# Kernel tuning notes

Hardware: AMD Instinct MI355X
Metric: run time of the kernel (lower is better)

## Reference

```python
import jax, jax.numpy as jnp
import numpy as np

H, W, C = 512, 512, 21
D_BI, D_SP = 5, 2
THETA_ALPHA, THETA_BETA, THETA_GAMMA = 80.0, 13.0, 3.0
BILATERAL_COMPAT, SPATIAL_COMPAT, COMPAT = 10.0, 3.0, -1.0
NUM_ITER = 5


def _build_lattice(feats):
    # Permutohedral lattice construction (Adams et al. 2010), vectorized numpy.
    # feats: [N, d] float64 -> (offsets [N,d+1] int32 into M lattice points,
    # barycentric weights [N,d+1] float32, blur_neighbors [d+1, M, 2] int32 (+1, 0=missing)).
    N, d = feats.shape
    scale = (np.sqrt(2.0 / 3.0) * (d + 1)) / np.sqrt((np.arange(d) + 1.0) * (np.arange(d) + 2.0))
    cf = feats * scale                                            # [N, d]
    S = np.concatenate([np.cumsum(cf[:, ::-1], axis=1)[:, ::-1], np.zeros((N, 1))], axis=1)
    elev = np.empty((N, d + 1))
    elev[:, 0] = S[:, 0]
    elev[:, 1:] = S[:, 1:] - np.arange(1, d + 1) * cf             # embed on H_d hyperplane
    rem0 = np.floor(elev / (d + 1) + 0.5) * (d + 1)               # nearest 0-colored point
    sums = np.rint(rem0.sum(1) / (d + 1)).astype(np.int64)
    diff = elev - rem0
    idx = np.arange(d + 1)
    gt = diff[:, None, :] > diff[:, :, None]
    eq = (diff[:, None, :] == diff[:, :, None]) & (idx[None, None, :] < idx[None, :, None])
    rank = (gt | eq).sum(2).astype(np.int64) + sums[:, None]
    lo = rank < 0
    rank += (d + 1) * lo
    rem0 += (d + 1) * lo
    hi = rank > d
    rank -= (d + 1) * hi
    rem0 -= (d + 1) * hi
    v = (elev - rem0) / (d + 1)
    b = np.zeros((N, d + 2))
    rows = np.arange(N)[:, None]
    np.add.at(b, (rows, d - rank), v)
    np.add.at(b, (rows, d + 1 - rank), -v)
    b[:, 0] += 1.0 + b[:, d + 1]
    ws = b[:, :d + 1].astype(np.float32)                          # weight per remainder r
    rem0i = np.rint(rem0[:, :d]).astype(np.int64)
    r = np.arange(d + 1)
    keys = rem0i[:, None, :] + r[None, :, None] - (d + 1) * (rank[:, None, :d] > (d - r)[None, :, None])
    uniq, os_flat = np.unique(keys.reshape(-1, d), axis=0, return_inverse=True)
    M = uniq.shape[0]
    os_ = os_flat.reshape(N, d + 1).astype(np.int32)
    n1 = np.repeat(uniq[None] + 1, d + 1, axis=0)                 # [d+1, M, d]
    n2 = np.repeat(uniq[None] - 1, d + 1, axis=0)
    for j in range(d):
        n1[j, :, j] = uniq[:, j] - d
        n2[j, :, j] = uniq[:, j] + d
    allk = np.concatenate([uniq, n1.reshape(-1, d), n2.reshape(-1, d)], axis=0)
    _, inv = np.unique(allk, axis=0, return_inverse=True)
    lut = np.full(int(inv.max()) + 1, -1, np.int64)
    lut[inv[:M]] = np.arange(M)
    i1 = lut[inv[M:M + (d + 1) * M]].reshape(d + 1, M)
    i2 = lut[inv[M + (d + 1) * M:]].reshape(d + 1, M)
    bn = (np.stack([i1, i2], axis=-1) + 1).astype(np.int32)       # 0 == missing neighbor
    return os_, ws, bn


def setup_inputs():
    key = jax.random.key(0)
    k1, k2 = jax.random.split(key)
    unary = jax.random.normal(k1, (H, W, C), jnp.float32)
    # piecewise-constant random image (realistic local color coherence)
    base = np.asarray(jax.random.uniform(k2, (32, 32, 3)), dtype=np.float64) * 255.0
    image = np.kron(base, np.ones((H // 32, W // 32, 1)))
    yy, xx = np.mgrid[0:H, 0:W].astype(np.float64)
    bi = np.concatenate([np.stack([xx / THETA_ALPHA, yy / THETA_ALPHA], -1),
                         image / THETA_BETA], axis=-1).reshape(-1, D_BI)
    sp = np.stack([xx / THETA_GAMMA, yy / THETA_GAMMA], -1).reshape(-1, D_SP)
    os_b, ws_b, bn_b = _build_lattice(bi)
    os_s, ws_s, bn_s = _build_lattice(sp)
    return {'unary': unary,
            'ws_b': jnp.asarray(ws_b), 'ws_s': jnp.asarray(ws_s),
            'os_b': jnp.asarray(os_b), 'os_s': jnp.asarray(os_s),
            'bn_b': jnp.asarray(bn_b), 'bn_s': jnp.asarray(bn_s)}


def _filter(Q, os_, ws, bn, alpha):
    # splat -> blur -> slice over one permutohedral lattice
    M = bn.shape[1]
    vals = jnp.zeros((M + 1, Q.shape[-1]), Q.dtype)
    vals = vals.at[os_ + 1].add(ws[:, :, None] * Q[:, None, :])   # splat (row 0 = pad)
    for j in range(bn.shape[0]):                                  # blur along d+1 lattice axes
        vals = vals.at[1:].add(0.5 * (vals[bn[j, :, 0]] + vals[bn[j, :, 1]]))
    return alpha * jnp.einsum('nj,njc->nc', ws, vals[os_ + 1])    # slice


def reference(unary, ws_b, ws_s, os_b, os_s, bn_b, bn_s):
    U = unary.reshape(-1, unary.shape[-1])                        # [N, C]
    a_b = 1.0 / (1.0 + 2.0 ** (-D_BI))
    a_s = 1.0 / (1.0 + 2.0 ** (-D_SP))
    ones = jnp.ones((U.shape[0], 1), U.dtype)
    inv_nb = 1.0 / (_filter(ones, os_b, ws_b, bn_b, a_b) + 1e-20)
    inv_ns = 1.0 / (_filter(ones, os_s, ws_s, bn_s, a_s) + 1e-20)
    Q = jax.nn.softmax(-U, axis=-1)
    for _ in range(NUM_ITER):
        msg = BILATERAL_COMPAT * (_filter(Q, os_b, ws_b, bn_b, a_b) * inv_nb) \
            + SPATIAL_COMPAT * (_filter(Q, os_s, ws_s, bn_s, a_s) * inv_ns)
        Q = jax.nn.softmax(-U - COMPAT * msg, axis=-1)
    return Q.reshape(unary.shape)
```

## Files before the change

kernel.cpp:

```cpp
#include <hip/hip_runtime.h>
#include <hip/hip_fp16.h>

#define NCH 21
#define NCH2 22
#define VSH 32
#define QSH 32
#define NPIX (512*512)
#define DECODE (1.0f/(16383.f*128.f))

__device__ __forceinline__ int wave_rank_atomic(int m, bool valid, int* __restrict__ cur) {
  int lane = threadIdx.x & 63;
  unsigned long long todo = __ballot(valid);
  int out = 0;
  while (todo) {
    int leader = __ffsll((unsigned long long)todo) - 1;
    int lm = __shfl(m, leader);
    unsigned long long match = __ballot(valid && (m == lm));
    int cnt = __popcll(match);
    int b = 0;
    if (lane == leader) b = atomicAdd(&cur[lm], cnt);
    b = __shfl(b, leader);
    if (valid && (m == lm)) {
      int rank = __popcll(match & ((1ull << lane) - 1ull));
      out = b + rank;
    }
    todo &= ~match;
  }
  return out;
}


__global__ void count_fused_kernel(const int* __restrict__ os_b, const int* __restrict__ os_s,
                                   int* __restrict__ cnt, int npb, int nptot, int Mb) {
  int t = blockIdx.x*blockDim.x + threadIdx.x;
  bool valid = (t < nptot);
  int m = 0;
  if (valid) m = (t < npb) ? os_b[t] : (Mb + os_s[t - npb]);
  int lane = threadIdx.x & 63;
  unsigned long long todo = __ballot(valid);
  while (todo) {
    int leader = __ffsll((unsigned long long)todo) - 1;
    int lm = __shfl(m, leader);
    unsigned long long match = __ballot(valid && (m == lm));
    if (lane == leader) atomicAdd(&cnt[lm], __popcll(match));
    todo &= ~match;
  }
}

__global__ void scan_block_kernel(const int* __restrict__ cnt, int* __restrict__ excl,
                                  int* __restrict__ bsum, int M) {
  __shared__ int s[256];
  int i = blockIdx.x*256 + threadIdx.x;
  int v = (i < M) ? cnt[i] : 0;
  s[threadIdx.x] = v;
  __syncthreads();
  for (int off = 1; off < 256; off <<= 1) {
    int t = (threadIdx.x >= off) ? s[threadIdx.x - off] : 0;
    __syncthreads();
    s[threadIdx.x] += t;
    __syncthreads();
  }
  if (i < M) excl[i] = s[threadIdx.x] - v;
  if (threadIdx.x == 255) bsum[blockIdx.x] = s[255];
}

__global__ void scan_sums_kernel(int* __restrict__ bsum, int nb) {
  __shared__ int s[256];
  __shared__ int carry;
  if (threadIdx.x == 0) carry = 0;
  __syncthreads();
  for (int base = 0; base < nb; base += 256) {
    int i = base + threadIdx.x;
    int v = (i < nb) ? bsum[i] : 0;
    s[threadIdx.x] = v;
    __syncthreads();
    for (int off = 1; off < 256; off <<= 1) {
      int t = (threadIdx.x >= off) ? s[threadIdx.x - off] : 0;
      __syncthreads();
      s[threadIdx.x] += t;
      __syncthreads();
    }
    if (i < nb) bsum[i] = s[threadIdx.x] - v + carry;
    int tot = s[255];
    __syncthreads();
    if (threadIdx.x == 0) carry += tot;
    __syncthreads();
  }
}

__global__ void scan_add_kernel(int* __restrict__ excl, const int* __restrict__ bsum,
                                int M, int nptot) {
  int i = blockIdx.x*blockDim.x + threadIdx.x;
  if (i < M) excl[i] += bsum[i >> 8];
  else if (i == M) excl[M] = nptot;
}

__global__ void fill_fused_kernel(const int* __restrict__ os_b, const float* __restrict__ ws_b,
                                  const int* __restrict__ os_s, const float* __restrict__ ws_s,
                                  const int* __restrict__ start, int* __restrict__ cur,
                                  unsigned int* __restrict__ pw, int npb, int nptot, int Mb) {
  int t = blockIdx.x*blockDim.x + threadIdx.x;
  bool valid = (t < nptot);
  int m = 0, pix = 0; float w = 0.f;
  if (valid) {
    if (t < npb) { m = os_b[t]; pix = t / 6; w = ws_b[t]; }
    else { int t2 = t - npb; m = Mb + os_s[t2]; pix = t2 / 3; w = ws_s[t2]; }
  }
  int slot = wave_rank_atomic(m, valid, cur);
  if (valid) {
    int w14 = (int)(w * 16383.f + 0.5f);
    w14 = w14 < 0 ? 0 : (w14 > 16383 ? 16383 : w14);
    pw[start[m] + slot] = ((unsigned int)pix << 14) | (unsigned int)w14;
  }
}


__global__ void gather_wave_kernel(const __half* __restrict__ Qh, const int* __restrict__ start,
                                   const unsigned int* __restrict__ pw,
                                   __half* __restrict__ valsB, __half* __restrict__ valsS,
                                   int Mb, int Mtot) {
  int wid = blockIdx.x*(blockDim.x >> 6) + (threadIdx.x >> 6);
  if (wid >= Mtot) return;
  int lane = threadIdx.x & 63;
  int pg = lane / 21;
  int c  = lane - pg*21;
  float s = 0.f, wsum = 0.f;
  int k1 = start[wid+1];
  if (pg < 3) {
    int k = start[wid] + pg;
    for (; k + 9 < k1; k += 12) {
      unsigned int a0 = pw[k], a1 = pw[k+3], a2 = pw[k+6], a3 = pw[k+9];
      float w0 = (float)(a0 & 16383u), w1 = (float)(a1 & 16383u);
      float w2 = (float)(a2 & 16383u), w3 = (float)(a3 & 16383u);
      s += w0 * __half2float(Qh[((size_t)(a0 >> 14) << 5) + c])
         + w1 * __half2float(Qh[((size_t)(a1 >> 14) << 5) + c])
         + w2 * __half2float(Qh[((size_t)(a2 >> 14) << 5) + c])
         + w3 * __half2float(Qh[((size_t)(a3 >> 14) << 5) + c]);
      wsum += w0 + w1 + w2 + w3;
    }
    for (; k < k1; k += 3) {
      unsigned int a = pw[k];
      float w = (float)(a & 16383u);
      s += w * __half2float(Qh[((size_t)(a >> 14) << 5) + c]);
      wsum += w;
    }
  }
  float s1 = __shfl(s, (lane + 21) & 63);
  float s2 = __shfl(s, (lane + 42) & 63);
  float wt = __shfl(wsum, 0) + __shfl(wsum, 21) + __shfl(wsum, 42);
  __half* row = (wid < Mb) ? (valsB + (size_t)(wid+1)*VSH)
                           : (valsS + (size_t)(wid-Mb+1)*VSH);
  if (lane < 21)       row[c]  = __float2half((s + s1 + s2) * DECODE);
  else if (lane == 21) row[21] = __float2half(wt * DECODE);
}

__global__ void blurH_fused_kernel(const __half* __restrict__ inB, __half* __restrict__ outB,
                                   const int* __restrict__ bnB, int Mb,
                                   const __half* __restrict__ inS, __half* __restrict__ outS,
                                   const int* __restrict__ bnS, int Ms) {
  int t = blockIdx.x*blockDim.x + threadIdx.x;
  const __half* in; __half* out; const int* bn; int i, j;
  int tb = Mb*11;
  if (t < tb) { i = t/11; j = t - i*11; in = inB; out = outB; bn = bnB; }
  else {
    int t2 = t - tb;
    if (t2 >= Ms*11) return;
    i = t2/11; j = t2 - i*11; in = inS; out = outS; bn = bnS;
  }
  int b0 = bn[2*i], b1 = bn[2*i+1];
  float2 a = __half22float2(((const __half2*)(in + (size_t)(i+1)*VSH))[j]);
  float2 x = __half22float2(((const __half2*)(in + (size_t)b0*VSH))[j]);
  float2 y = __half22float2(((const __half2*)(in + (size_t)b1*VSH))[j]);
  float2 o;
  o.x = a.x + 0.5f*(x.x + y.x);
  o.y = a.y + 0.5f*(x.y + y.y);
  ((__half2*)(out + (size_t)(i+1)*VSH))[j] = __float22half2_rn(o);
}


__global__ void softmax_init_kernel(const float* __restrict__ U, __half* __restrict__ Qh) {
  int n = blockIdx.x*blockDim.x + threadIdx.x;
  if (n >= NPIX) return;
  float l[NCH];
  float m = -3.4e38f;
  #pragma unroll
  for (int c = 0; c < NCH; ++c) { l[c] = -U[(size_t)n*NCH+c]; m = fmaxf(m, l[c]); }
  float s = 0.f;
  #pragma unroll
  for (int c = 0; c < NCH; ++c) { l[c] = expf(l[c]-m); s += l[c]; }
  float r = 1.0f/s;
  #pragma unroll
  for (int c = 0; c < NCH; ++c) Qh[(size_t)n*QSH+c] = __float2half(l[c]*r);
}

template<bool FINAL>
__global__ void slice_combine_softmax_kernel(
    const float* __restrict__ U,
    const __half* __restrict__ vb, const __half* __restrict__ vs,
    const float* __restrict__ ws_b, const int* __restrict__ os_b,
    const float* __restrict__ ws_s, const int* __restrict__ os_s,
    float* __restrict__ QoutF, __half* __restrict__ QoutH) {
  int n = blockIdx.x*blockDim.x + threadIdx.x;
  if (n >= NPIX) return;
  float l[NCH];
  #pragma unroll
  for (int c = 0; c < NCH; ++c) l[c] = -U[(size_t)n*NCH+c];
  float acc[NCH2];
  #pragma unroll
  for (int c = 0; c < NCH2; ++c) acc[c] = 0.f;
  #pragma unroll
  for (int j = 0; j < 6; ++j) {
    float w = ws_b[n*6+j];
    const __half* v = vb + (size_t)(os_b[n*6+j]+1)*VSH;
    #pragma unroll
    for (int c = 0; c < NCH2; ++c) acc[c] += w*__half2float(v[c]);
  }
  float rb = 10.0f/(acc[NCH] + 1e-12f);
  #pragma unroll
  for (int c = 0; c < NCH; ++c) l[c] += rb*acc[c];
  #pragma unroll
  for (int c = 0; c < NCH2; ++c) acc[c] = 0.f;
  #pragma unroll
  for (int j = 0; j < 3; ++j) {
    float w = ws_s[n*3+j];
    const __half* v = vs + (size_t)(os_s[n*3+j]+1)*VSH;
    #pragma unroll
    for (int c = 0; c < NCH2; ++c) acc[c] += w*__half2float(v[c]);
  }
  float rs = 3.0f/(acc[NCH] + 1e-12f);
  #pragma unroll
  for (int c = 0; c < NCH; ++c) l[c] += rs*acc[c];
  float m = -3.4e38f;
  #pragma unroll
  for (int c = 0; c < NCH; ++c) m = fmaxf(m, l[c]);
  float s = 0.f;
  #pragma unroll
  for (int c = 0; c < NCH; ++c) { l[c] = expf(l[c]-m); s += l[c]; }
  float r = 1.0f/s;
  if (FINAL) {
    #pragma unroll
    for (int c = 0; c < NCH; ++c) QoutF[(size_t)n*NCH+c] = l[c]*r;
  } else {
    #pragma unroll
    for (int c = 0; c < NCH; ++c) QoutH[(size_t)n*QSH+c] = __float2half(l[c]*r);
  }
}


extern "C" void kernel_launch(void* const* d_in, const int* in_sizes, int n_in,
                              void* d_out, int out_size, void* d_ws, size_t ws_size,
                              hipStream_t stream) {
  const float* U    = (const float*)d_in[0];
  const float* ws_b = (const float*)d_in[1];
  const float* ws_s = (const float*)d_in[2];
  const int*   os_b = (const int*)d_in[3];
  const int*   os_s = (const int*)d_in[4];
  const int*   bn_b = (const int*)d_in[5];
  const int*   bn_s = (const int*)d_in[6];
  const int Mb = in_sizes[5] / 12;
  const int Ms = in_sizes[6] / 6;
  const int Mtot = Mb + Ms;
  const int npb = NPIX*6, nps = NPIX*3;
  const int nptot = npb + nps;

  char* wcur = (char*)d_ws;
  auto alloc = [&](size_t bytes) -> void* {
    void* p = (void*)wcur;
    wcur += (bytes + 63) & ~(size_t)63;
    return p;
  };
  __half* Qh    = (__half*)alloc((size_t)NPIX*QSH*2);
  __half* vAb   = (__half*)alloc((size_t)(Mb+1)*VSH*2);
  __half* vBb   = (__half*)alloc((size_t)(Mb+1)*VSH*2);
  __half* vAs   = (__half*)alloc((size_t)(Ms+1)*VSH*2);
  __half* vBs   = (__half*)alloc((size_t)(Ms+1)*VSH*2);
  int*   start  = (int*)alloc((size_t)(Mtot+1)*4);
  int*   cur    = (int*)alloc((size_t)Mtot*4);
  unsigned int* pw = (unsigned int*)alloc((size_t)nptot*4);
  int*   bsum   = (int*)alloc((size_t)(Mtot/256 + 2)*4);

  const int TB = 256;
  auto blocks = [](long long n){ return (int)((n + 255)/256); };

  hipMemsetAsync(cur, 0, (size_t)Mtot*sizeof(int), stream);
  count_fused_kernel<<<blocks(nptot), TB, 0, stream>>>(os_b, os_s, cur, npb, nptot, Mb);
  scan_block_kernel<<<blocks(Mtot), 256, 0, stream>>>(cur, start, bsum, Mtot);
  scan_sums_kernel<<<1, 256, 0, stream>>>(bsum, blocks(Mtot));
  scan_add_kernel<<<blocks(Mtot+1), TB, 0, stream>>>(start, bsum, Mtot, nptot);
  hipMemsetAsync(cur, 0, (size_t)Mtot*sizeof(int), stream);
  fill_fused_kernel<<<blocks(nptot), TB, 0, stream>>>(os_b, ws_b, os_s, ws_s,
                                                      start, cur, pw, npb, nptot, Mb);

  hipMemsetAsync(vAb, 0, VSH*2, stream);
  hipMemsetAsync(vBb, 0, VSH*2, stream);
  hipMemsetAsync(vAs, 0, VSH*2, stream);
  hipMemsetAsync(vBs, 0, VSH*2, stream);

  softmax_init_kernel<<<blocks(NPIX), TB, 0, stream>>>(U, Qh);

  for (int it = 0; it < 5; ++it) {
    gather_wave_kernel<<<blocks((long long)Mtot*64), TB, 0, stream>>>(
        Qh, start, pw, vAb, vAs, Mb, Mtot);
    __half* ab = vAb; __half* bb = vBb;
    __half* as = vAs; __half* bs = vBs;
    for (int j = 0; j < 6; ++j) {
      int ms = (j < 3) ? Ms : 0;
      blurH_fused_kernel<<<blocks((long long)(Mb + ms)*11), TB, 0, stream>>>(
          ab, bb, bn_b + (size_t)j*Mb*2, Mb, as, bs, bn_s + (size_t)j*Ms*2, ms);
      { __half* t = ab; ab = bb; bb = t; }
      if (j < 3) { __half* t = as; as = bs; bs = t; }
    }
    if (it == 4) {
      slice_combine_softmax_kernel<true><<<blocks(NPIX), TB, 0, stream>>>(
          U, ab, as, ws_b, os_b, ws_s, os_s, (float*)d_out, (__half*)nullptr);
    } else {
      slice_combine_softmax_kernel<false><<<blocks(NPIX), TB, 0, stream>>>(
          U, ab, as, ws_b, os_b, ws_s, os_s, (float*)nullptr, Qh);
    }
  }
}
```

Baseline: 491.3 us.

## Split long lattice splat lists into fixed segments and cache unary as fp16

Gather work is split into segments of at most 192 entries per wave. Per-segment float partials are written out, and a new combine kernel sums them per lattice point, so heavily populated points no longer serialize on one wave. The fill and count kernels now walk entries in vertex-major order, so consecutive threads handle consecutive pixels for the same vertex. The softmax init also writes a padded fp16 copy of the negated unary, which cuts the per-iteration unary read bandwidth. In exchange it adds setup kernels (segment count, scan, fill), an extra combine pass each iteration, and lower unary precision.

Result: slower. 531.9 us (+8.3%).

```diff
diff --git a/kernel.cpp b/kernel.cpp
--- a/kernel.cpp
+++ b/kernel.cpp
@@ -5,7 +5,9 @@
 #define NCH2 22
 #define VSH 32
 #define QSH 32
+#define USH 24
 #define NPIX (512*512)
+#define SEG 192
 #define DECODE (1.0f/(16383.f*128.f))
 
 __device__ __forceinline__ int wave_rank_atomic(int m, bool valid, int* __restrict__ cur) {
@@ -20,10 +22,7 @@
     int b = 0;
     if (lane == leader) b = atomicAdd(&cur[lm], cnt);
     b = __shfl(b, leader);
-    if (valid && (m == lm)) {
-      int rank = __popcll(match & ((1ull << lane) - 1ull));
-      out = b + rank;
-    }
+    if (valid && (m == lm)) out = b + __popcll(match & ((1ull << lane) - 1ull));
     todo &= ~match;
   }
   return out;
@@ -31,11 +30,14 @@
 
 
 __global__ void count_fused_kernel(const int* __restrict__ os_b, const int* __restrict__ os_s,
-                                   int* __restrict__ cnt, int npb, int nptot, int Mb) {
+                                   int* __restrict__ cnt, int nptot, int Mb) {
   int t = blockIdx.x*blockDim.x + threadIdx.x;
   bool valid = (t < nptot);
   int m = 0;
-  if (valid) m = (t < npb) ? os_b[t] : (Mb + os_s[t - npb]);
+  if (valid) {
+    if (t < 6*NPIX) { int j = t >> 18, n = t & (NPIX-1); m = os_b[n*6+j]; }
+    else { int t2 = t - 6*NPIX; int j = t2 >> 18, n = t2 & (NPIX-1); m = Mb + os_s[n*3+j]; }
+  }
   int lane = threadIdx.x & 63;
   unsigned long long todo = __ballot(valid);
   while (todo) {
@@ -86,25 +88,27 @@
     if (threadIdx.x == 0) carry += tot;
     __syncthreads();
   }
+  if (threadIdx.x == 0) bsum[nb] = carry;
 }
 
 __global__ void scan_add_kernel(int* __restrict__ excl, const int* __restrict__ bsum,
-                                int M, int nptot) {
+                                int M, int nb) {
   int i = blockIdx.x*blockDim.x + threadIdx.x;
   if (i < M) excl[i] += bsum[i >> 8];
-  else if (i == M) excl[M] = nptot;
+  else if (i == M) excl[M] = bsum[nb];
 }
 
 __global__ void fill_fused_kernel(const int* __restrict__ os_b, const float* __restrict__ ws_b,
                                   const int* __restrict__ os_s, const float* __restrict__ ws_s,
                                   const int* __restrict__ start, int* __restrict__ cur,
-                                  unsigned int* __restrict__ pw, int npb, int nptot, int Mb) {
+                                  unsigned int* __restrict__ pw, int nptot, int Mb) {
   int t = blockIdx.x*blockDim.x + threadIdx.x;
   bool valid = (t < nptot);
   int m = 0, pix = 0; float w = 0.f;
   if (valid) {
-    if (t < npb) { m = os_b[t]; pix = t / 6; w = ws_b[t]; }
-    else { int t2 = t - npb; m = Mb + os_s[t2]; pix = t2 / 3; w = ws_s[t2]; }
+    if (t < 6*NPIX) { int j = t >> 18, n = t & (NPIX-1); m = os_b[n*6+j]; pix = n; w = ws_b[n*6+j]; }
+    else { int t2 = t - 6*NPIX; int j = t2 >> 18, n = t2 & (NPIX-1);
+           m = Mb + os_s[n*3+j]; pix = n; w = ws_s[n*3+j]; }
   }
   int slot = wave_rank_atomic(m, valid, cur);
   if (valid) {
@@ -115,19 +119,38 @@
 }
 
 
-__global__ void gather_wave_kernel(const __half* __restrict__ Qh, const int* __restrict__ start,
-                                   const unsigned int* __restrict__ pw,
-                                   __half* __restrict__ valsB, __half* __restrict__ valsS,
-                                   int Mb, int Mtot) {
+__global__ void nseg_kernel(const int* __restrict__ start, int* __restrict__ segcnt, int Mtot) {
+  int m = blockIdx.x*blockDim.x + threadIdx.x;
+  if (m >= Mtot) return;
+  int len = start[m+1] - start[m];
+  segcnt[m] = (len + SEG - 1) / SEG;
+}
+
+__global__ void seg_fill_kernel(const int* __restrict__ segstart, int* __restrict__ seg_m, int Mtot) {
+  int m = blockIdx.x*blockDim.x + threadIdx.x;
+  if (m >= Mtot) return;
+  int b = segstart[m], e = segstart[m+1];
+  for (int s = b; s < e; ++s) seg_m[s] = m;
+}
+
+
+__global__ void gather_seg_kernel(const __half* __restrict__ Qh, const int* __restrict__ start,
+                                  const int* __restrict__ segstart, const int* __restrict__ seg_m,
+                                  const unsigned int* __restrict__ pw,
+                                  float* __restrict__ partials, int Mtot) {
   int wid = blockIdx.x*(blockDim.x >> 6) + (threadIdx.x >> 6);
-  if (wid >= Mtot) return;
+  int NSEG = segstart[Mtot];
+  if (wid >= NSEG) return;
+  int m = seg_m[wid];
+  int k0 = start[m] + (wid - segstart[m])*SEG;
+  int k1 = start[m+1];
+  if (k1 > k0 + SEG) k1 = k0 + SEG;
   int lane = threadIdx.x & 63;
   int pg = lane / 21;
   int c  = lane - pg*21;
   float s = 0.f, wsum = 0.f;
-  int k1 = start[wid+1];
   if (pg < 3) {
-    int k = start[wid] + pg;
+    int k = k0 + pg;
     for (; k + 9 < k1; k += 12) {
       unsigned int a0 = pw[k], a1 = pw[k+3], a2 = pw[k+6], a3 = pw[k+9];
       float w0 = (float)(a0 & 16383u), w1 = (float)(a1 & 16383u);
@@ -148,10 +171,27 @@
   float s1 = __shfl(s, (lane + 21) & 63);
   float s2 = __shfl(s, (lane + 42) & 63);
   float wt = __shfl(wsum, 0) + __shfl(wsum, 21) + __shfl(wsum, 42);
-  __half* row = (wid < Mb) ? (valsB + (size_t)(wid+1)*VSH)
-                           : (valsS + (size_t)(wid-Mb+1)*VSH);
-  if (lane < 21)       row[c]  = __float2half((s + s1 + s2) * DECODE);
-  else if (lane == 21) row[21] = __float2half(wt * DECODE);
+  float* row = partials + (size_t)wid*NCH2;
+  if (lane < 21)       row[c]  = s + s1 + s2;
+  else if (lane == 21) row[21] = wt;
+}
+
+__global__ void combine_kernel(const float* __restrict__ partials,
+                               const int* __restrict__ segstart,
+                               __half* __restrict__ valsB, __half* __restrict__ valsS,
+                               int Mb, int Mtot) {
+  int t = blockIdx.x*blockDim.x + threadIdx.x;
+  if (t >= Mtot*NCH2) return;
+  int m = t / NCH2, c = t - m*NCH2;
+  int s0 = segstart[m], s1 = segstart[m+1];
+  float acc = 0.f;
+  int s = s0;
+  for (; s + 3 < s1; s += 4)
+    acc += partials[(size_t)s*NCH2+c] + partials[(size_t)(s+1)*NCH2+c]
+         + partials[(size_t)(s+2)*NCH2+c] + partials[(size_t)(s+3)*NCH2+c];
+  for (; s < s1; ++s) acc += partials[(size_t)s*NCH2+c];
+  __half* row = (m < Mb) ? (valsB + (size_t)(m+1)*VSH) : (valsS + (size_t)(m-Mb+1)*VSH);
+  row[c] = __float2half(acc * DECODE);
 }
 
 __global__ void blurH_fused_kernel(const __half* __restrict__ inB, __half* __restrict__ outB,
@@ -178,13 +218,18 @@
 }
 
 
-__global__ void softmax_init_kernel(const float* __restrict__ U, __half* __restrict__ Qh) {
+__global__ void softmax_init_kernel(const float* __restrict__ U, __half* __restrict__ Qh,
+                                    __half* __restrict__ Uh) {
   int n = blockIdx.x*blockDim.x + threadIdx.x;
   if (n >= NPIX) return;
   float l[NCH];
   float m = -3.4e38f;
   #pragma unroll
-  for (int c = 0; c < NCH; ++c) { l[c] = -U[(size_t)n*NCH+c]; m = fmaxf(m, l[c]); }
+  for (int c = 0; c < NCH; ++c) {
+    l[c] = -U[(size_t)n*NCH+c];
+    Uh[(size_t)n*USH+c] = __float2half(l[c]);
+    m = fmaxf(m, l[c]);
+  }
   float s = 0.f;
   #pragma unroll
   for (int c = 0; c < NCH; ++c) { l[c] = expf(l[c]-m); s += l[c]; }
@@ -195,7 +240,7 @@
 
 template<bool FINAL>
 __global__ void slice_combine_softmax_kernel(
-    const float* __restrict__ U,
+    const __half* __restrict__ Uh,
     const __half* __restrict__ vb, const __half* __restrict__ vs,
     const float* __restrict__ ws_b, const int* __restrict__ os_b,
     const float* __restrict__ ws_s, const int* __restrict__ os_s,
@@ -204,7 +249,7 @@
   if (n >= NPIX) return;
   float l[NCH];
   #pragma unroll
-  for (int c = 0; c < NCH; ++c) l[c] = -U[(size_t)n*NCH+c];
+  for (int c = 0; c < NCH; ++c) l[c] = __half2float(Uh[(size_t)n*USH+c]);
   float acc[NCH2];
   #pragma unroll
   for (int c = 0; c < NCH2; ++c) acc[c] = 0.f;
@@ -260,8 +305,8 @@
   const int Mb = in_sizes[5] / 12;
   const int Ms = in_sizes[6] / 6;
   const int Mtot = Mb + Ms;
-  const int npb = NPIX*6, nps = NPIX*3;
-  const int nptot = npb + nps;
+  const int nptot = NPIX*9;
+  const int nseg_max = Mtot + nptot/SEG + 2;
 
   char* wcur = (char*)d_ws;
   auto alloc = [&](size_t bytes) -> void* {
@@ -269,38 +314,51 @@
     wcur += (bytes + 63) & ~(size_t)63;
     return p;
   };
-  __half* Qh    = (__half*)alloc((size_t)NPIX*QSH*2);
-  __half* vAb   = (__half*)alloc((size_t)(Mb+1)*VSH*2);
-  __half* vBb   = (__half*)alloc((size_t)(Mb+1)*VSH*2);
-  __half* vAs   = (__half*)alloc((size_t)(Ms+1)*VSH*2);
-  __half* vBs   = (__half*)alloc((size_t)(Ms+1)*VSH*2);
-  int*   start  = (int*)alloc((size_t)(Mtot+1)*4);
-  int*   cur    = (int*)alloc((size_t)Mtot*4);
+  __half* Qh     = (__half*)alloc((size_t)NPIX*QSH*2);
+  __half* Uh     = (__half*)alloc((size_t)NPIX*USH*2);
+  __half* vAb    = (__half*)alloc((size_t)(Mb+1)*VSH*2);
+  __half* vBb    = (__half*)alloc((size_t)(Mb+1)*VSH*2);
+  __half* vAs    = (__half*)alloc((size_t)(Ms+1)*VSH*2);
+  __half* vBs    = (__half*)alloc((size_t)(Ms+1)*VSH*2);
+  int*   start   = (int*)alloc((size_t)(Mtot+1)*4);
+  int*   cur     = (int*)alloc((size_t)Mtot*4);
+  int*   segstart= (int*)alloc((size_t)(Mtot+1)*4);
+  int*   seg_m   = (int*)alloc((size_t)nseg_max*4);
   unsigned int* pw = (unsigned int*)alloc((size_t)nptot*4);
-  int*   bsum   = (int*)alloc((size_t)(Mtot/256 + 2)*4);
+  float* partials= (float*)alloc((size_t)nseg_max*NCH2*4);
+  int*   bsum    = (int*)alloc((size_t)(Mtot/256 + 3)*4);
 
   const int TB = 256;
   auto blocks = [](long long n){ return (int)((n + 255)/256); };
+  const int nbM = blocks(Mtot);
 
   hipMemsetAsync(cur, 0, (size_t)Mtot*sizeof(int), stream);
-  count_fused_kernel<<<blocks(nptot), TB, 0, stream>>>(os_b, os_s, cur, npb, nptot, Mb);
-  scan_block_kernel<<<blocks(Mtot), 256, 0, stream>>>(cur, start, bsum, Mtot);
-  scan_sums_kernel<<<1, 256, 0, stream>>>(bsum, blocks(Mtot));
-  scan_add_kernel<<<blocks(Mtot+1), TB, 0, stream>>>(start, bsum, Mtot, nptot);
+  count_fused_kernel<<<blocks(nptot), TB, 0, stream>>>(os_b, os_s, cur, nptot, Mb);
+  scan_block_kernel<<<nbM, 256, 0, stream>>>(cur, start, bsum, Mtot);
+  scan_sums_kernel<<<1, 256, 0, stream>>>(bsum, nbM);
+  scan_add_kernel<<<blocks(Mtot+1), TB, 0, stream>>>(start, bsum, Mtot, nbM);
   hipMemsetAsync(cur, 0, (size_t)Mtot*sizeof(int), stream);
   fill_fused_kernel<<<blocks(nptot), TB, 0, stream>>>(os_b, ws_b, os_s, ws_s,
-                                                      start, cur, pw, npb, nptot, Mb);
+                                                      start, cur, pw, nptot, Mb);
+
+  nseg_kernel<<<nbM, TB, 0, stream>>>(start, cur, Mtot);
+  scan_block_kernel<<<nbM, 256, 0, stream>>>(cur, segstart, bsum, Mtot);
+  scan_sums_kernel<<<1, 256, 0, stream>>>(bsum, nbM);
+  scan_add_kernel<<<blocks(Mtot+1), TB, 0, stream>>>(segstart, bsum, Mtot, nbM);
+  seg_fill_kernel<<<nbM, TB, 0, stream>>>(segstart, seg_m, Mtot);
 
   hipMemsetAsync(vAb, 0, VSH*2, stream);
   hipMemsetAsync(vBb, 0, VSH*2, stream);
   hipMemsetAsync(vAs, 0, VSH*2, stream);
   hipMemsetAsync(vBs, 0, VSH*2, stream);
 
-  softmax_init_kernel<<<blocks(NPIX), TB, 0, stream>>>(U, Qh);
+  softmax_init_kernel<<<blocks(NPIX), TB, 0, stream>>>(U, Qh, Uh);
 
   for (int it = 0; it < 5; ++it) {
-    gather_wave_kernel<<<blocks((long long)Mtot*64), TB, 0, stream>>>(
-        Qh, start, pw, vAb, vAs, Mb, Mtot);
+    gather_seg_kernel<<<blocks((long long)nseg_max*64), TB, 0, stream>>>(
+        Qh, start, segstart, seg_m, pw, partials, Mtot);
+    combine_kernel<<<blocks((long long)Mtot*NCH2), TB, 0, stream>>>(
+        partials, segstart, vAb, vAs, Mb, Mtot);
     __half* ab = vAb; __half* bb = vBb;
     __half* as = vAs; __half* bs = vBs;
     for (int j = 0; j < 6; ++j) {
@@ -312,10 +370,10 @@
     }
     if (it == 4) {
       slice_combine_softmax_kernel<true><<<blocks(NPIX), TB, 0, stream>>>(
-          U, ab, as, ws_b, os_b, ws_s, os_s, (float*)d_out, (__half*)nullptr);
+          Uh, ab, as, ws_b, os_b, ws_s, os_s, (float*)d_out, (__half*)nullptr);
     } else {
       slice_combine_softmax_kernel<false><<<blocks(NPIX), TB, 0, stream>>>(
-          U, ab, as, ws_b, os_b, ws_s, os_s, (float*)nullptr, Qh);
-    }
-  }
-}
+          Uh, ab, as, ws_b, os_b, ws_s, os_s, (float*)nullptr, Qh);
+    }
+  }
+}
```
